# Optimization experiments

Hardware: AMD Instinct MI355X
Metric: run time of the kernel (lower is better)

## Reference

```python
import jax, jax.numpy as jnp
import numpy as np

B, S, HOPS, DIM, NREL = 1024, 32, 2, 64, 237
NENT, NEDGE = 14541, 272115
SIGMA = 0.1
CFMW = 64


def setup_inputs() -> dict:
    key = jax.random.key(0)
    ks = jax.random.split(key, 20)

    def g(k, shape):
        return (jax.random.normal(k, shape, dtype=jnp.float32) / np.float32(np.sqrt(shape[0])))

    inp = {
        "entity_pairs": jax.random.randint(ks[0], (B, 2), 0, NENT),
        "train_edges": jax.random.randint(ks[1], (B,), 0, NEDGE),
        "labels": jax.random.randint(ks[2], (B,), 0, NREL),
        "entity2edges": jax.random.randint(ks[3], (NENT + 1, S), 0, NEDGE + 1),
        "edge2entities": jax.random.randint(ks[4], (NEDGE + 1, 1), 0, NENT + 1),
        "edge2relation": jax.random.randint(ks[5], (NEDGE + 1,), 0, NREL + 1),
        "t": jax.random.uniform(ks[6], (B,), dtype=jnp.float32),
        "eps": jax.random.normal(ks[7], (B, NREL), dtype=jnp.float32),
        "rel_feat": g(ks[8], (NREL, DIM)),
        "W_agg0": g(ks[9], (DIM, DIM)), "b_agg0": jnp.zeros((DIM,), jnp.float32),
        "W_agg1": g(ks[10], (DIM, NREL)), "b_agg1": jnp.zeros((NREL,), jnp.float32),
        "W_out": g(ks[11], (2 * NREL, NREL)), "b_out": jnp.zeros((NREL,), jnp.float32),
        "mW1": g(ks[12], (NREL + 1, CFMW)), "mb1": jnp.zeros((CFMW,), jnp.float32),
        "mW2": g(ks[13], (CFMW, CFMW)), "mb2": jnp.zeros((CFMW,), jnp.float32),
        "mW3": g(ks[14], (CFMW, CFMW)), "mb3": jnp.zeros((CFMW,), jnp.float32),
        "mW4": g(ks[15], (CFMW, NREL)), "mb4": jnp.zeros((NREL,), jnp.float32),
    }
    return inp


def _side(ent, labels, train_edges, entity2edges, edge2entities, edge2relation, relf, aggs):
    # multi-hop neighbor edge gather + masks (exclude the training edge itself)
    edges_list = [labels]  # hop-0 "edges" are the relation labels
    masks = []
    for i in range(HOPS):
        if i == 0:
            ne = ent.reshape(B, 1)  # (B, 1) source entities
        else:
            ne = edge2entities[edges_list[-1].reshape(-1)].reshape(B, -1)
        nedges = entity2edges[ne.reshape(-1)].reshape(B, -1)  # (B, S**(i+1))
        edges_list.append(nedges)
        masks.append((nedges != train_edges[:, None]).astype(relf.dtype))
    # edge -> relation -> feature
    ev = [relf[edges_list[0]]]  # (B, DIM)
    for edges in edges_list[1:]:
        ev.append(relf[edge2relation[edges]])  # (B, S**h, DIM)
    # iterative mean aggregation (PathCon-style, one entity per edge)
    for i in range(HOPS):
        W, b, act, self_inc = aggs[i]
        d = W.shape[0]
        nxt = []
        for hop in range(HOPS - i):
            neigh = ev[hop + 1].reshape(B, -1, 1, S, d)
            m = masks[hop].reshape(B, -1, 1, S, 1)
            out = jnp.mean(jnp.mean(neigh * m, axis=-2), axis=-2)  # (B, S**hop, d)
            if self_inc:
                out = out + ev[hop].reshape(B, -1, d)
            nxt.append(act(out @ W + b))
        ev = nxt
    return ev[0].reshape(B, NREL)


def reference(entity_pairs, train_edges, labels, entity2edges, edge2entities,
              edge2relation, t, eps, rel_feat, W_agg0, b_agg0, W_agg1, b_agg1,
              W_out, b_out, mW1, mb1, mW2, mb2, mW3, mb3, mW4, mb4):
    relf = jnp.concatenate([rel_feat, jnp.zeros((1, DIM), rel_feat.dtype)], axis=0)
    aggs = [
        (W_agg0, b_agg0, jax.nn.relu, True),    # intermediate hop: relu, self-included
        (W_agg1, b_agg1, lambda x: x, False),   # last hop: identity, no self
    ]
    x0 = _side(entity_pairs[:, 0], labels, train_edges, entity2edges,
               edge2entities, edge2relation, relf, aggs)
    x1 = _side(entity_pairs[:, 1], labels, train_edges, entity2edges,
               edge2entities, edge2relation, relf, aggs)
    output = jnp.concatenate([x0, x1], axis=-1) @ W_out + b_out  # (B, NREL)
    # CFM: xt = (1-t) x0 + t x1 + sigma*eps ; ut = x1 - x0
    tb = t[:, None]
    xt = (1.0 - tb) * x0 + tb * x1 + SIGMA * eps
    h = jnp.concatenate([xt, tb], axis=-1)
    h = jax.nn.selu(h @ mW1 + mb1)
    h = jax.nn.selu(h @ mW2 + mb2)
    h = jax.nn.selu(h @ mW3 + mb3)
    vt = h @ mW4 + mb4
    scores = output * vt
    return scores
```

## Files before the change

### kernel.cpp

```cpp
#include <hip/hip_runtime.h>
#include <math.h>

#define BB 1024
#define S 32
#define DIM 64
#define NREL 237
#define NENT 14541
#define SIGMA 0.1f

#define OFS_WR    0
#define N_WR      (238*64)
#define OFS_WC0   15232
#define N_WC      (64*237)
#define OFS_WC1   (OFS_WC0 + N_WC)
#define OFS_BC    (OFS_WC1 + N_WC)
#define OFS_HC    (OFS_BC + 237)
#define OFS_A     45872

#define LDS_BYTES 18688

__device__ __forceinline__ float selu_f(float x) {
    const float alpha = 1.6732632423543772f;
    const float scale = 1.0507009873554805f;
    return scale * (x > 0.f ? x : alpha * expm1f(x));
}

__global__ __launch_bounds__(256) void pre_wr_kernel(
    const float* __restrict__ rel_feat, const float* __restrict__ W0,
    float* __restrict__ ws) {
    int idx = blockIdx.x * 256 + threadIdx.x;
    if (idx < 238 * 64) {
        int r = idx >> 6, o = idx & 63;
        float acc = 0.f;
        if (r < NREL) {
#pragma unroll 8
            for (int d = 0; d < 64; ++d)
                acc += rel_feat[r * 64 + d] * W0[d * 64 + o];
        }
        ws[OFS_WR + idx] = acc;
    }
}

__global__ __launch_bounds__(512) void mid_kernel(
    const int* __restrict__ e2e_tab, const int* __restrict__ e2r,
    const float* __restrict__ W1, const float* __restrict__ b1,
    const float* __restrict__ W_out, const float* __restrict__ b_out,
    const float* __restrict__ mW1, const float* __restrict__ mb1,
    float* __restrict__ ws) {
    __shared__ int   s_r[1024];
    __shared__ float red[512];
    int blk = blockIdx.x;
    const int tid = threadIdx.x;

    if (blk < 455) {
        const int grp = tid >> 4, c = tid & 15;
        const int ent = blk * 32 + grp;
        const bool ok = ent < (NENT + 1);
        if (ok) {
            int ea = e2e_tab[ent * S + c];
            int eb = e2e_tab[ent * S + 16 + c];
            s_r[grp * 32 + c] = e2r[ea];
            s_r[grp * 32 + 16 + c] = e2r[eb];
        }
        __syncthreads();
        if (ok) {
            const float4* Wr4 = (const float4*)(ws + OFS_WR);
            const int* rr = &s_r[grp * 32];
            float4 acc = make_float4(0.f, 0.f, 0.f, 0.f);
#pragma unroll
            for (int s = 0; s < 32; ++s) {
                float4 v = Wr4[rr[s] * 16 + c];
                acc.x += v.x; acc.y += v.y; acc.z += v.z; acc.w += v.w;
            }
            ((float4*)(ws + OFS_A))[ent * 16 + c] = acc;
        }
        return;
    }
    blk -= 455;
    if (blk < 512) {
        int half = blk >> 8;
        int lb = blk & 255;
        int o = lb >> 2, ct = lb & 3;
        int cl = tid & 63, q = tid >> 6;
        int c = ct * 64 + cl;
        const float* Wsrc = W_out + half * 237 * 237;
        float acc = 0.f;
        if (c < NREL) {
            int k0 = q * 30, k1 = (q == 7) ? 237 : (k0 + 30);
#pragma unroll 4
            for (int k = k0; k < k1; ++k)
                acc += W1[o * 237 + k] * Wsrc[k * 237 + c];
        }
        red[tid] = acc;
        __syncthreads();
        if (q == 0 && c < NREL) {
            float s = 0.f;
#pragma unroll
            for (int qq = 0; qq < 8; ++qq) s += red[qq * 64 + cl];
            ws[(half ? OFS_WC1 : OFS_WC0) + o * 237 + c] = s;
        }
        return;
    }
    blk -= 512;
    if (blk < 4) {
        int cl = tid & 63, q = tid >> 6;
        int c = blk * 64 + cl;
        float acc = 0.f;
        if (c < NREL) {
            int k0 = q * 30, k1 = (q == 7) ? 237 : (k0 + 30);
#pragma unroll 4
            for (int k = k0; k < k1; ++k)
                acc += b1[k] * (W_out[k * 237 + c] + W_out[(237 + k) * 237 + c]);
        }
        red[tid] = acc;
        __syncthreads();
        if (q == 0 && c < NREL) {
            float s = b_out[c];
#pragma unroll
            for (int qq = 0; qq < 8; ++qq) s += red[qq * 64 + cl];
            ws[OFS_BC + c] = s;
        }
        return;
    }
    {
        int w = tid & 63, q = tid >> 6;
        int k0 = q * 30, k1 = (q == 7) ? 237 : (k0 + 30);
        float acc = 0.f;
#pragma unroll 4
        for (int k = k0; k < k1; ++k)
            acc += b1[k] * mW1[k * 64 + w];
        red[tid] = acc;
        __syncthreads();
        if (q == 0) {
            float s = mb1[w];
#pragma unroll
            for (int qq = 0; qq < 8; ++qq) s += red[qq * 64 + w];
            ws[OFS_HC + w] = s;
        }
    }
}

__global__ __launch_bounds__(512, 8) void gf_kernel(
    const int* __restrict__ ep, const int* __restrict__ te_arr,
    const int* __restrict__ e2e_tab, const int* __restrict__ e2ent,
    const int* __restrict__ e2r, const float* __restrict__ b0,
    const float* __restrict__ t_arr, const float* __restrict__ eps,
    const float* __restrict__ W1, const float* __restrict__ mW1,
    const float* __restrict__ mW2, const float* __restrict__ mb2,
    const float* __restrict__ mW3, const float* __restrict__ mb3,
    const float* __restrict__ mW4, const float* __restrict__ mb4,
    const float* __restrict__ ws, float* __restrict__ out) {
    extern __shared__ float smem[];
    float* s_v1   = smem;
    int*   s_r1   = (int*)(smem + 4352);
    int*   s_ent2 = (int*)(smem + 4416);
    float* s_m1   = smem + 4480;
    float* s_ov   = smem + 4544;

    const int tid = threadIdx.x;
    const int b = blockIdx.x;
    const int grp = tid >> 4;
    const int c = tid & 15;
    const int te = te_arr[b];
    const int rte = e2r[te];
    const float4* Wr4 = (const float4*)(ws + OFS_WR);
    const float4* A4  = (const float4*)(ws + OFS_A);
    const float4 b0v  = ((const float4*)b0)[c];
    const float4 wrte = Wr4[rte * 16 + c];

    if (tid < 64) {
        int u = tid >> 5, s = tid & 31;
        int ent = ep[b * 2 + u];
        int e1 = e2e_tab[ent * S + s];
        s_r1[u * 32 + s] = e2r[e1];
        s_m1[u * 32 + s] = (e1 != te) ? 1.0f : 0.0f;
        s_ent2[u * 32 + s] = e2ent[e1];
    }
    __syncthreads();

    const float inv = 1.0f / 32.0f;
#pragma unroll
    for (int u = 0; u < 2; ++u) {
        const int j = grp;
        const int ent2 = s_ent2[u * 32 + j];
        int e2a = e2e_tab[ent2 * S + c];
        int e2b = e2e_tab[ent2 * S + 16 + c];
        int cnt = (e2a == te) + (e2b == te);
        cnt += __shfl_xor(cnt, 1);
        cnt += __shfl_xor(cnt, 2);
        cnt += __shfl_xor(cnt, 4);
        cnt += __shfl_xor(cnt, 8);
        float4 a4   = A4[ent2 * 16 + c];
        float4 self = Wr4[s_r1[u * 32 + j] * 16 + c];
        float fc = (float)cnt;
        float m = s_m1[u * 32 + j];
        float4 r;
        r.x = fmaxf(self.x + (a4.x - fc * wrte.x) * inv + b0v.x, 0.f) * m;
        r.y = fmaxf(self.y + (a4.y - fc * wrte.y) * inv + b0v.y, 0.f) * m;
        r.z = fmaxf(self.z + (a4.z - fc * wrte.z) * inv + b0v.z, 0.f) * m;
        r.w = fmaxf(self.w + (a4.w - fc * wrte.w) * inv + b0v.w, 0.f) * m;
        *((float4*)&s_v1[(u * 32 + j) * 68 + c * 4]) = r;
    }
    __syncthreads();
    if (tid < 128) {
        int u = tid >> 6, w = tid & 63;
        float sum = 0.f;
#pragma unroll 8
        for (int j = 0; j < 32; ++j) sum += s_v1[(u * 32 + j) * 68 + w];
        s_ov[u * 64 + w] = sum * inv;
    }
    __syncthreads();

    float* s_ymix = smem;
    float* s_outv = smem + 240;
    float* s_red  = smem + 480;
    float* s_h    = smem + 992;
    float* s_omix = smem + 1056;
    float* s_vp   = smem + 1120;
    const float tb = t_arr[b];
    const float* Wc0 = ws + OFS_WC0;
    const float* Wc1 = ws + OFS_WC1;
    const float* bc = ws + OFS_BC;
    const float* hc = ws + OFS_HC;

    if (tid < 64)
        s_omix[tid] = (1.f - tb) * s_ov[tid] + tb * s_ov[64 + tid];
    __syncthreads();

    if (tid < 256) {
        if (tid < NREL) {
            float y = 0.f;
#pragma unroll 4
            for (int d = 0; d < 64; ++d)
                y += s_omix[d] * W1[d * 237 + tid];
            s_ymix[tid] = y;
        }
    } else {
        int cc = tid - 256;
        if (cc < NREL) {
            float a = bc[cc];
#pragma unroll 4
            for (int d = 0; d < 64; ++d)
                a += s_ov[d] * Wc0[d * 237 + cc] + s_ov[64 + d] * Wc1[d * 237 + cc];
            s_outv[cc] = a;
        }
    }
    __syncthreads();

    {
        int w = tid & 63, q = tid >> 6;
        int k0 = q * 30, k1 = (q == 7) ? 237 : (k0 + 30);
        const float* e = eps + b * 237;
        float a = 0.f;
#pragma unroll 4
        for (int k = k0; k < k1; ++k)
            a += (SIGMA * e[k] + s_ymix[k]) * mW1[k * 64 + w];
        s_red[tid] = a;
    }
    __syncthreads();
    if (tid < 64) {
        float h = hc[tid] + tb * mW1[237 * 64 + tid];
#pragma unroll
        for (int q = 0; q < 8; ++q) h += s_red[q * 64 + tid];
        s_h[tid] = selu_f(h);
    }
    __syncthreads();

    {
        int w = tid & 63, q = tid >> 6;
        float a = 0.f;
#pragma unroll
        for (int d = q * 8; d < q * 8 + 8; ++d)
            a += s_h[d] * mW2[d * 64 + w];
        s_red[tid] = a;
    }
    __syncthreads();
    if (tid < 64) {
        float v = mb2[tid];
#pragma unroll
        for (int q = 0; q < 8; ++q) v += s_red[q * 64 + tid];
        s_h[tid] = selu_f(v);
    }
    __syncthreads();

    {
        int w = tid & 63, q = tid >> 6;
        float a = 0.f;
#pragma unroll
        for (int d = q * 8; d < q * 8 + 8; ++d)
            a += s_h[d] * mW3[d * 64 + w];
        s_red[tid] = a;
    }
    __syncthreads();
    if (tid < 64) {
        float v = mb3[tid];
#pragma unroll
        for (int q = 0; q < 8; ++q) v += s_red[q * 64 + tid];
        s_h[tid] = selu_f(v);
    }
    __syncthreads();

    {
        int half = tid >> 8, cc = tid & 255;
        if (cc < NREL) {
            float a = 0.f;
#pragma unroll 4
            for (int w = half * 32; w < half * 32 + 32; ++w)
                a += s_h[w] * mW4[w * 237 + cc];
            s_vp[half * 240 + cc] = a;
        }
    }
    __syncthreads();
    if (tid < NREL)
        out[b * 237 + tid] = s_outv[tid] * (mb4[tid] + s_vp[tid] + s_vp[240 + tid]);
}

extern "C" void kernel_launch(void* const* d_in, const int* in_sizes, int n_in,
                              void* d_out, int out_size, void* d_ws, size_t ws_size,
                              hipStream_t stream) {
    const int* ep       = (const int*)d_in[0];
    const int* te       = (const int*)d_in[1];
    const int* e2e      = (const int*)d_in[3];
    const int* e2ent    = (const int*)d_in[4];
    const int* e2r      = (const int*)d_in[5];
    const float* t      = (const float*)d_in[6];
    const float* eps    = (const float*)d_in[7];
    const float* relf   = (const float*)d_in[8];
    const float* W0     = (const float*)d_in[9];
    const float* b0     = (const float*)d_in[10];
    const float* W1     = (const float*)d_in[11];
    const float* b1     = (const float*)d_in[12];
    const float* W_out  = (const float*)d_in[13];
    const float* b_out  = (const float*)d_in[14];
    const float* mW1    = (const float*)d_in[15];
    const float* mb1    = (const float*)d_in[16];
    const float* mW2    = (const float*)d_in[17];
    const float* mb2    = (const float*)d_in[18];
    const float* mW3    = (const float*)d_in[19];
    const float* mb3    = (const float*)d_in[20];
    const float* mW4    = (const float*)d_in[21];
    const float* mb4    = (const float*)d_in[22];
    float* ws  = (float*)d_ws;
    float* out = (float*)d_out;

    hipLaunchKernelGGL(pre_wr_kernel, dim3(60), dim3(256), 0, stream,
                       relf, W0, ws);
    hipLaunchKernelGGL(mid_kernel, dim3(972), dim3(512), 0, stream,
                       e2e, e2r, W1, b1, W_out, b_out, mW1, mb1, ws);
    hipLaunchKernelGGL(gf_kernel, dim3(BB), dim3(512), LDS_BYTES, stream,
                       ep, te, e2e, e2ent, e2r, b0,
                       t, eps, W1, mW1, mW2, mb2, mW3, mb3, mW4, mb4, ws, out);
}
```

Measured before the change: 139.9 us.

## Fold W_agg1 into first CFM layer and precompute per-sample eps projection

Precomputes Wm = W_agg1 @ mW1 (64x64) and a per-sample projection (sigma*eps + b1) @ mW1 + mb1 in the mid kernel. The per-block MLP's first layer then becomes a 64-wide dot instead of a 237-wide one. It also splits the output projection across both thread halves and runs the small 64x64 layers on 64 threads without reduction syncs. This removes the ymix stage and several barriers from the per-sample kernel, at the cost of extra precompute blocks and a workspace round trip.

```diff
diff --git a/kernel.cpp b/kernel.cpp
--- a/kernel.cpp
+++ b/kernel.cpp
@@ -14,8 +14,9 @@
 #define N_WC      (64*237)
 #define OFS_WC1   (OFS_WC0 + N_WC)
 #define OFS_BC    (OFS_WC1 + N_WC)
-#define OFS_HC    (OFS_BC + 237)
 #define OFS_A     45872
+#define OFS_WM    976560
+#define OFS_PE    980656
 
 #define LDS_BYTES 18688
 
@@ -46,6 +47,7 @@
     const float* __restrict__ W1, const float* __restrict__ b1,
     const float* __restrict__ W_out, const float* __restrict__ b_out,
     const float* __restrict__ mW1, const float* __restrict__ mb1,
+    const float* __restrict__ eps,
     float* __restrict__ ws) {
     __shared__ int   s_r[1024];
     __shared__ float red[512];
@@ -122,21 +124,26 @@
         }
         return;
     }
+    blk -= 4;
+    if (blk < 8) {
+        int idx = blk * 512 + tid;
+        int o = idx >> 6, c = idx & 63;
+        float acc = 0.f;
+#pragma unroll 4
+        for (int k = 0; k < 237; ++k)
+            acc += W1[o * 237 + k] * mW1[k * 64 + c];
+        ws[OFS_WM + idx] = acc;
+        return;
+    }
+    blk -= 8;
     {
-        int w = tid & 63, q = tid >> 6;
-        int k0 = q * 30, k1 = (q == 7) ? 237 : (k0 + 30);
-        float acc = 0.f;
-#pragma unroll 4
-        for (int k = k0; k < k1; ++k)
-            acc += b1[k] * mW1[k * 64 + w];
-        red[tid] = acc;
-        __syncthreads();
-        if (q == 0) {
-            float s = mb1[w];
-#pragma unroll
-            for (int qq = 0; qq < 8; ++qq) s += red[qq * 64 + w];
-            ws[OFS_HC + w] = s;
-        }
+        int b = blk * 8 + (tid >> 6), w = tid & 63;
+        const float* e = eps + b * 237;
+        float acc = mb1[w];
+#pragma unroll 4
+        for (int k = 0; k < 237; ++k)
+            acc += (SIGMA * e[k] + b1[k]) * mW1[k * 64 + w];
+        ws[OFS_PE + b * 64 + w] = acc;
     }
 }
 
@@ -144,8 +151,8 @@
     const int* __restrict__ ep, const int* __restrict__ te_arr,
     const int* __restrict__ e2e_tab, const int* __restrict__ e2ent,
     const int* __restrict__ e2r, const float* __restrict__ b0,
-    const float* __restrict__ t_arr, const float* __restrict__ eps,
-    const float* __restrict__ W1, const float* __restrict__ mW1,
+    const float* __restrict__ t_arr,
+    const float* __restrict__ mW1,
     const float* __restrict__ mW2, const float* __restrict__ mb2,
     const float* __restrict__ mW3, const float* __restrict__ mb3,
     const float* __restrict__ mW4, const float* __restrict__ mb4,
@@ -211,92 +218,71 @@
     }
     __syncthreads();
 
-    float* s_ymix = smem;
-    float* s_outv = smem + 240;
-    float* s_red  = smem + 480;
-    float* s_h    = smem + 992;
-    float* s_omix = smem + 1056;
-    float* s_vp   = smem + 1120;
+    float* s_outp = smem;
+    float* s_vp   = smem + 480;
+    float* s_hA   = smem + 960;
+    float* s_hB   = smem + 1024;
+    float* s_omix = smem + 1088;
     const float tb = t_arr[b];
     const float* Wc0 = ws + OFS_WC0;
     const float* Wc1 = ws + OFS_WC1;
-    const float* bc = ws + OFS_BC;
-    const float* hc = ws + OFS_HC;
+    const float* bc  = ws + OFS_BC;
+    const float* Wm  = ws + OFS_WM;
+    const float* pe  = ws + OFS_PE + b * 64;
 
     if (tid < 64)
         s_omix[tid] = (1.f - tb) * s_ov[tid] + tb * s_ov[64 + tid];
-    __syncthreads();
-
-    if (tid < 256) {
-        if (tid < NREL) {
-            float y = 0.f;
+    {
+        int half = tid >> 8, cc = tid & 255;
+        if (cc < NREL) {
+            const float* Wc  = half ? Wc1 : Wc0;
+            const float* ovp = s_ov + half * 64;
+            float a = 0.f;
 #pragma unroll 4
             for (int d = 0; d < 64; ++d)
-                y += s_omix[d] * W1[d * 237 + tid];
-            s_ymix[tid] = y;
-        }
-    } else {
-        int cc = tid - 256;
-        if (cc < NREL) {
-            float a = bc[cc];
-#pragma unroll 4
-            for (int d = 0; d < 64; ++d)
-                a += s_ov[d] * Wc0[d * 237 + cc] + s_ov[64 + d] * Wc1[d * 237 + cc];
-            s_outv[cc] = a;
-        }
-    }
-    __syncthreads();
-
-    {
-        int w = tid & 63, q = tid >> 6;
-        int k0 = q * 30, k1 = (q == 7) ? 237 : (k0 + 30);
-        const float* e = eps + b * 237;
-        float a = 0.f;
-#pragma unroll 4
-        for (int k = k0; k < k1; ++k)
-            a += (SIGMA * e[k] + s_ymix[k]) * mW1[k * 64 + w];
-        s_red[tid] = a;
-    }
-    __syncthreads();
+                a += ovp[d] * Wc[d * 237 + cc];
+            s_outp[half * 240 + cc] = a;
+        }
+    }
+    __syncthreads();
+
     if (tid < 64) {
-        float h = hc[tid] + tb * mW1[237 * 64 + tid];
-#pragma unroll
-        for (int q = 0; q < 8; ++q) h += s_red[q * 64 + tid];
-        s_h[tid] = selu_f(h);
-    }
-    __syncthreads();
-
-    {
-        int w = tid & 63, q = tid >> 6;
-        float a = 0.f;
-#pragma unroll
-        for (int d = q * 8; d < q * 8 + 8; ++d)
-            a += s_h[d] * mW2[d * 64 + w];
-        s_red[tid] = a;
-    }
-    __syncthreads();
+        float a0 = pe[tid] + tb * mW1[237 * 64 + tid];
+        float a1 = 0.f, a2 = 0.f, a3 = 0.f;
+#pragma unroll
+        for (int d = 0; d < 64; d += 4) {
+            a0 += s_omix[d]     * Wm[d * 64 + tid];
+            a1 += s_omix[d + 1] * Wm[(d + 1) * 64 + tid];
+            a2 += s_omix[d + 2] * Wm[(d + 2) * 64 + tid];
+            a3 += s_omix[d + 3] * Wm[(d + 3) * 64 + tid];
+        }
+        s_hA[tid] = selu_f((a0 + a1) + (a2 + a3));
+    }
+    __syncthreads();
+
     if (tid < 64) {
-        float v = mb2[tid];
-#pragma unroll
-        for (int q = 0; q < 8; ++q) v += s_red[q * 64 + tid];
-        s_h[tid] = selu_f(v);
-    }
-    __syncthreads();
-
-    {
-        int w = tid & 63, q = tid >> 6;
-        float a = 0.f;
-#pragma unroll
-        for (int d = q * 8; d < q * 8 + 8; ++d)
-            a += s_h[d] * mW3[d * 64 + w];
-        s_red[tid] = a;
-    }
-    __syncthreads();
+        float a0 = mb2[tid], a1 = 0.f, a2 = 0.f, a3 = 0.f;
+#pragma unroll
+        for (int d = 0; d < 64; d += 4) {
+            a0 += s_hA[d]     * mW2[d * 64 + tid];
+            a1 += s_hA[d + 1] * mW2[(d + 1) * 64 + tid];
+            a2 += s_hA[d + 2] * mW2[(d + 2) * 64 + tid];
+            a3 += s_hA[d + 3] * mW2[(d + 3) * 64 + tid];
+        }
+        s_hB[tid] = selu_f((a0 + a1) + (a2 + a3));
+    }
+    __syncthreads();
+
     if (tid < 64) {
-        float v = mb3[tid];
-#pragma unroll
-        for (int q = 0; q < 8; ++q) v += s_red[q * 64 + tid];
-        s_h[tid] = selu_f(v);
+        float a0 = mb3[tid], a1 = 0.f, a2 = 0.f, a3 = 0.f;
+#pragma unroll
+        for (int d = 0; d < 64; d += 4) {
+            a0 += s_hB[d]     * mW3[d * 64 + tid];
+            a1 += s_hB[d + 1] * mW3[(d + 1) * 64 + tid];
+            a2 += s_hB[d + 2] * mW3[(d + 2) * 64 + tid];
+            a3 += s_hB[d + 3] * mW3[(d + 3) * 64 + tid];
+        }
+        s_hA[tid] = selu_f((a0 + a1) + (a2 + a3));
     }
     __syncthreads();
 
@@ -306,13 +292,16 @@
             float a = 0.f;
 #pragma unroll 4
             for (int w = half * 32; w < half * 32 + 32; ++w)
-                a += s_h[w] * mW4[w * 237 + cc];
+                a += s_hA[w] * mW4[w * 237 + cc];
             s_vp[half * 240 + cc] = a;
         }
     }
     __syncthreads();
-    if (tid < NREL)
-        out[b * 237 + tid] = s_outv[tid] * (mb4[tid] + s_vp[tid] + s_vp[240 + tid]);
+
+    if (tid < NREL) {
+        float outv = bc[tid] + s_outp[tid] + s_outp[240 + tid];
+        out[b * 237 + tid] = outv * (mb4[tid] + s_vp[tid] + s_vp[240 + tid]);
+    }
 }
 
 extern "C" void kernel_launch(void* const* d_in, const int* in_sizes, int n_in,
@@ -345,9 +334,9 @@
 
     hipLaunchKernelGGL(pre_wr_kernel, dim3(60), dim3(256), 0, stream,
                        relf, W0, ws);
-    hipLaunchKernelGGL(mid_kernel, dim3(972), dim3(512), 0, stream,
-                       e2e, e2r, W1, b1, W_out, b_out, mW1, mb1, ws);
+    hipLaunchKernelGGL(mid_kernel, dim3(1107), dim3(512), 0, stream,
+                       e2e, e2r, W1, b1, W_out, b_out, mW1, mb1, eps, ws);
     hipLaunchKernelGGL(gf_kernel, dim3(BB), dim3(512), LDS_BYTES, stream,
                        ep, te, e2e, e2ent, e2r, b0,
-                       t, eps, W1, mW1, mW2, mb2, mW3, mb3, mW4, mb4, ws, out);
-}
+                       t, mW1, mW2, mb2, mW3, mb3, mW4, mb4, ws, out);
+}
```

After: 162.0 us. 15.8% more time.
